# Kernel optimization log

Hardware: AMD Instinct MI355X
Metric: run time of the kernel (lower is better)

## Reference

```python
import jax, jax.numpy as jnp
import numpy as np

D_IN = 2048
D_OUT = 2048
NUM_HEADS = 16
HEAD_DIM = D_OUT // NUM_HEADS


def setup_inputs() -> dict:
    key = jax.random.key(0)
    k_x, k_qkv, k_proj, k_b = jax.random.split(key, 4)
    x = jax.random.normal(k_x, (2, 2048, D_IN), dtype=jnp.float32)
    # torch Linear(d_in, 3*d_out, bias=False): weight [3*d_out, d_in]; store transposed [d_in, 3*d_out]
    Wqkv = jax.random.normal(k_qkv, (D_IN, 3 * D_OUT), dtype=jnp.float32) / np.sqrt(D_IN)
    Wproj = jax.random.normal(k_proj, (D_OUT, D_OUT), dtype=jnp.float32) / np.sqrt(D_OUT)
    bproj = jax.random.normal(k_b, (D_OUT,), dtype=jnp.float32) * 0.01
    return {"x": x, "Wqkv": Wqkv, "Wproj": Wproj, "bproj": bproj}


def reference(x, Wqkv, Wproj, bproj):
    B, S, _ = x.shape
    qkv = x @ Wqkv  # [B, S, 3*D_OUT]
    qkv = qkv.reshape(B, S, 3, NUM_HEADS, HEAD_DIM)
    qkv = jnp.transpose(qkv, (2, 0, 3, 1, 4))  # [3, B, H, S, Dh]
    q, k, v = qkv[0], qkv[1], qkv[2]
    scale = 1.0 / np.sqrt(HEAD_DIM).astype(np.float32)
    scores = jnp.einsum('bhqd,bhkd->bhqk', q, k) * scale  # [B, H, S, S]
    causal = jnp.tril(jnp.ones((S, S), dtype=bool))
    scores = jnp.where(causal, scores, jnp.finfo(scores.dtype).min)
    attn = jax.nn.softmax(scores, axis=-1)
    out = jnp.einsum('bhqk,bhkd->bhqd', attn, v)  # [B, H, S, Dh]
    out = jnp.transpose(out, (0, 2, 1, 3)).reshape(B, S, D_OUT)
    return out @ Wproj + bproj
```

## Files before the change

kernel.cpp:

```cpp
#include <hip/hip_runtime.h>
#include <stdint.h>

typedef __attribute__((ext_vector_type(8))) short short8;
typedef __attribute__((ext_vector_type(4))) float f32x4;
typedef __attribute__((ext_vector_type(16))) float f32x16;
typedef __attribute__((ext_vector_type(4))) unsigned short u16x4;

typedef unsigned short u16;

constexpr int S_LEN = 2048;
constexpr int DH    = 128;

__device__ __forceinline__ u16 f2bf(float f) {
    union { float f; unsigned u; } v; v.f = f;
    unsigned r = v.u + 0x7FFFu + ((v.u >> 16) & 1u);
    return (u16)(r >> 16);
}
__device__ __forceinline__ void gl_lds16(const void* g, void* l) {
    __builtin_amdgcn_global_load_lds((const __attribute__((address_space(1))) void*)g,
                                     (__attribute__((address_space(3))) void*)l,
                                     16, 0, 0);
}

__global__ __launch_bounds__(256) void convx(const float* __restrict__ src,
                                             u16* __restrict__ dst) {
    size_t i = ((size_t)blockIdx.x * 256 + threadIdx.x) * 8;
    f32x4 a = *(const f32x4*)(src + i);
    f32x4 b = *(const f32x4*)(src + i + 4);
    short8 r;
    r[0] = (short)f2bf(a[0]); r[1] = (short)f2bf(a[1]);
    r[2] = (short)f2bf(a[2]); r[3] = (short)f2bf(a[3]);
    r[4] = (short)f2bf(b[0]); r[5] = (short)f2bf(b[1]);
    r[6] = (short)f2bf(b[2]); r[7] = (short)f2bf(b[3]);
    *(short8*)(dst + i) = r;
}

__global__ void convT(const float* __restrict__ src, u16* __restrict__ dst,
                      int rows, int cols) {
    __shared__ u16 tile[32][33];
    int c0 = blockIdx.x * 32, r0 = blockIdx.y * 32;
    int tx = threadIdx.x, ty = threadIdx.y;
#pragma unroll
    for (int i = 0; i < 32; i += 8)
        tile[ty + i][tx] = f2bf(src[(size_t)(r0 + ty + i) * cols + c0 + tx]);
    __syncthreads();
#pragma unroll
    for (int i = 0; i < 32; i += 8)
        dst[(size_t)(c0 + ty + i) * rows + r0 + tx] = tile[tx][ty + i];
}

__global__ __launch_bounds__(512, 2) void gemm_qkv(
        const u16* __restrict__ A, const u16* __restrict__ BT,
        u16* __restrict__ Qo, u16* __restrict__ Ko, u16* __restrict__ VTo) {
    __shared__ __align__(16) u16 lA[2][128 * 64];
    __shared__ __align__(16) u16 lB[2][256 * 64];
    const int tid = threadIdx.x;
    const int lane = tid & 63, wave = tid >> 6;
    const int quad = lane >> 4, l16 = lane & 15;
    const int wr = wave >> 2, wc = wave & 3;
    const int m0 = blockIdx.y * 128, n0 = blockIdx.x * 256;
    const int sw = l16 & 7;
    const int c4 = tid & 7;
    f32x4 acc[4][4] = {};

    auto stageA = [&](int t1, int nb) {
#pragma unroll
        for (int j = 0; j < 2; ++j) {
            int idx = j * 512 + tid;
            int row = idx >> 3;
            gl_lds16(A + (size_t)(m0 + row) * 2048 + t1 * 64 + ((c4 ^ (row & 7)) * 8),
                     &lA[nb][row * 64 + c4 * 8]);
        }
    };
    auto stageB = [&](int h, int t1, int nb) {
#pragma unroll
        for (int j = 0; j < 2; ++j) {
            int rih = (j * 512 + tid) >> 3;
            int row = (rih & 31) + h * 32 + (rih >> 5) * 64;
            gl_lds16(BT + (size_t)(n0 + row) * 2048 + t1 * 64 + ((c4 ^ (row & 7)) * 8),
                     &lB[nb][row * 64 + c4 * 8]);
        }
    };

    stageA(0, 0); stageB(0, 0, 0); stageB(1, 0, 0);

    constexpr int NT = 32;
    for (int t = 0; t < NT; ++t) {
        const int buf = t & 1, nb = buf ^ 1;
        const bool pf = (t + 1 < NT);
        asm volatile("s_waitcnt vmcnt(2)\n\ts_barrier" ::: "memory");
        short8 af[4][2], bf0[2][2];
        const int abase = (wr * 64 + l16) * 64;
        const int bbase = (wc * 64 + l16) * 64;
#pragma unroll
        for (int m = 0; m < 4; ++m)
#pragma unroll
            for (int ks = 0; ks < 2; ++ks)
                af[m][ks] = *(const short8*)&lA[buf][abase + m * 1024 + (((ks * 4 + quad) ^ sw)) * 8];
#pragma unroll
        for (int n = 0; n < 2; ++n)
#pragma unroll
            for (int ks = 0; ks < 2; ++ks)
                bf0[n][ks] = *(const short8*)&lB[buf][bbase + n * 1024 + (((ks * 4 + quad) ^ sw)) * 8];
        if (pf) { stageA(t + 1, nb); stageB(0, t + 1, nb); }
        __builtin_amdgcn_s_setprio(1);
#pragma unroll
        for (int m = 0; m < 4; ++m)
#pragma unroll
            for (int n = 0; n < 2; ++n)
#pragma unroll
                for (int ks = 0; ks < 2; ++ks)
                    acc[m][n] = __builtin_amdgcn_mfma_f32_16x16x32_bf16(
                        af[m][ks], bf0[n][ks], acc[m][n], 0, 0, 0);
        __builtin_amdgcn_s_setprio(0);
        if (pf) asm volatile("s_waitcnt vmcnt(4)\n\ts_barrier" ::: "memory");
        else    asm volatile("s_waitcnt vmcnt(0)\n\ts_barrier" ::: "memory");
        short8 bf1[2][2];
#pragma unroll
        for (int n = 0; n < 2; ++n)
#pragma unroll
            for (int ks = 0; ks < 2; ++ks)
                bf1[n][ks] = *(const short8*)&lB[buf][bbase + 2048 + n * 1024 + (((ks * 4 + quad) ^ sw)) * 8];
        if (pf) stageB(1, t + 1, nb);
        __builtin_amdgcn_s_setprio(1);
#pragma unroll
        for (int m = 0; m < 4; ++m)
#pragma unroll
            for (int n = 0; n < 2; ++n)
#pragma unroll
                for (int ks = 0; ks < 2; ++ks)
                    acc[m][n + 2] = __builtin_amdgcn_mfma_f32_16x16x32_bf16(
                        af[m][ks], bf1[n][ks], acc[m][n + 2], 0, 0, 0);
        __builtin_amdgcn_s_setprio(0);
    }

#pragma unroll
    for (int m = 0; m < 4; ++m) {
        int r0r = m0 + wr * 64 + m * 16 + quad * 4;
        int b = r0r >> 11, s0 = r0r & 2047;
#pragma unroll
        for (int n = 0; n < 4; ++n) {
            int cc = n0 + wc * 64 + n * 16 + l16;
            int which = cc >> 11, hd = (cc >> 7) & 15, dh = cc & 127;
            if (which < 2) {
                u16* dst = which == 0 ? Qo : Ko;
#pragma unroll
                for (int rg = 0; rg < 4; ++rg)
                    dst[(size_t)((b * 16 + hd) * 2048 + s0 + rg) * 128 + dh] = f2bf(acc[m][n][rg]);
            } else {
                u16x4 v;
#pragma unroll
                for (int rg = 0; rg < 4; ++rg) v[rg] = f2bf(acc[m][n][rg]);
                *(u16x4*)&VTo[((size_t)(b * 16 + hd) * 128 + dh) * 2048 + s0] = v;
            }
        }
    }
}

__global__ __launch_bounds__(256, 2) void attn_kern(
        u16* __restrict__ QOp, const u16* __restrict__ Kp,
        const u16* __restrict__ VTp) {
    __shared__ __align__(16) u16 lK[2][64 * 128];
    __shared__ __align__(16) u16 lV[2][128 * 64];
    const int tid = threadIdx.x, lane = tid & 63, wave = tid >> 6;
    const int ql = lane & 31, hi = lane >> 5;
    const int qb = (blockIdx.y < 8) ? (15 - (int)blockIdx.y) : ((int)blockIdx.y - 8);
    const int bh = blockIdx.x;
    const int qbase = qb * 128 + wave * 32;
    const int qmax = qbase + 31;
    const int nkt = 2 * qb + 2;
    u16* Qh = QOp + (size_t)bh * S_LEN * DH;
    const u16* Kh = Kp + (size_t)bh * S_LEN * DH;
    const u16* VTh = VTp + (size_t)bh * DH * S_LEN;

    short8 qf[8];
#pragma unroll
    for (int c = 0; c < 8; ++c)
        qf[c] = *(const short8*)&Qh[(size_t)(qbase + ql) * 128 + c * 16 + hi * 8];

    f32x16 acc[4] = {};
    float mrun = -1e30f, lrun = 0.f;
    const float SC = 0.08838834764831845f * 1.44269504088896f;

    auto stage = [&](int kt, int b) {
        const u16* ks = Kh + (size_t)kt * 64 * 128;
#pragma unroll
        for (int p = 0; p < 4; ++p) {
            int slot = p * 256 + tid;
            int row = slot >> 4, c4 = slot & 15;
            gl_lds16(ks + row * 128 + ((c4 ^ (row & 15)) * 8), &lK[b][slot * 8]);
        }
        const u16* vs = VTh + kt * 64;
#pragma unroll
        for (int p = 0; p < 4; ++p) {
            int slot = p * 256 + tid;
            int row = slot >> 3, c4 = slot & 7;
            gl_lds16(vs + (size_t)row * 2048 + ((c4 ^ (row & 7)) * 8), &lV[b][slot * 8]);
        }
    };

    stage(0, 0);
    __syncthreads();

    for (int kt = 0; kt < nkt; ++kt) {
        const int buf = kt & 1;
        if (kt + 1 < nkt) stage(kt + 1, buf ^ 1);
        if (kt * 64 <= qmax) {
            const bool part = (kt * 64 + 63 > qbase);
            f32x16 s0 = {}, s1 = {};
            __builtin_amdgcn_s_setprio(1);
#pragma unroll
            for (int c = 0; c < 8; ++c) {
                int sl = ((c * 2 + hi) ^ (ql & 15)) * 8;
                short8 k0 = *(const short8*)&lK[buf][ql * 128 + sl];
                short8 k1 = *(const short8*)&lK[buf][(32 + ql) * 128 + sl];
                s0 = __builtin_amdgcn_mfma_f32_32x32x16_bf16(k0, qf[c], s0, 0, 0, 0);
                s1 = __builtin_amdgcn_mfma_f32_32x32x16_bf16(k1, qf[c], s1, 0, 0, 0);
            }
            __builtin_amdgcn_s_setprio(0);
            float pv0[16], pv1[16];
            float pm = -1e30f;
            const int qg = qbase + ql;
#pragma unroll
            for (int r = 0; r < 16; ++r) {
                int krow = (r & 3) + 8 * (r >> 2) + 4 * hi;
                float a = s0[r] * SC;
                float b = s1[r] * SC;
                if (part) {
                    if (kt * 64 + krow > qg)      a = -1e30f;
                    if (kt * 64 + 32 + krow > qg) b = -1e30f;
                }
                pv0[r] = a; pv1[r] = b;
                pm = fmaxf(pm, fmaxf(a, b));
            }
            pm = fmaxf(pm, __shfl_xor(pm, 32));
            if (__any(pm - mrun > 8.f)) {
                float mn = fmaxf(mrun, pm);
                float al = exp2f(mrun - mn);
                mrun = mn;
                lrun *= al;
#pragma unroll
                for (int r = 0; r < 16; ++r) {
                    float ar = __shfl(al, (r & 3) + 8 * (r >> 2) + 4 * hi);
#pragma unroll
                    for (int dc = 0; dc < 4; ++dc)
                        acc[dc][r] *= ar;
                }
            }
            float rs = 0.f;
#pragma unroll
            for (int r = 0; r < 16; ++r) {
                pv0[r] = exp2f(pv0[r] - mrun);
                pv1[r] = exp2f(pv1[r] - mrun);
                rs += pv0[r] + pv1[r];
            }
            rs += __shfl_xor(rs, 32);
            lrun += rs;
            unsigned X0[8], X1[8];
#pragma unroll
            for (int i = 0; i < 8; ++i) {
                X0[i] = (unsigned)f2bf(pv0[2 * i]) | ((unsigned)f2bf(pv0[2 * i + 1]) << 16);
                X1[i] = (unsigned)f2bf(pv1[2 * i]) | ((unsigned)f2bf(pv1[2 * i + 1]) << 16);
            }
            short8 pa[4];
#pragma unroll
            for (int t = 0; t < 2; ++t)
#pragma unroll
                for (int h = 0; h < 2; ++h) {
                    unsigned x0 = t ? X1[4 * h + 0] : X0[4 * h + 0];
                    unsigned x1 = t ? X1[4 * h + 1] : X0[4 * h + 1];
                    unsigned x2 = t ? X1[4 * h + 2] : X0[4 * h + 2];
                    unsigned x3 = t ? X1[4 * h + 3] : X0[4 * h + 3];
                    unsigned sx0 = (unsigned)__shfl_xor((int)x0, 32);
                    unsigned sx1 = (unsigned)__shfl_xor((int)x1, 32);
                    unsigned sx2 = (unsigned)__shfl_xor((int)x2, 32);
                    unsigned sx3 = (unsigned)__shfl_xor((int)x3, 32);
                    union { unsigned u[4]; short8 s; } uf;
                    uf.u[0] = hi ? sx2 : x0;
                    uf.u[1] = hi ? sx3 : x1;
                    uf.u[2] = hi ? x2 : sx0;
                    uf.u[3] = hi ? x3 : sx1;
                    pa[t * 2 + h] = uf.s;
                }
            __builtin_amdgcn_s_setprio(1);
#pragma unroll
            for (int dc = 0; dc < 4; ++dc) {
                const int rv = dc * 32 + ql;
#pragma unroll
                for (int kc = 0; kc < 4; ++kc) {
                    short8 vf = *(const short8*)&lV[buf][rv * 64 + (((kc * 2 + hi) ^ (ql & 7)) * 8)];
                    acc[dc] = __builtin_amdgcn_mfma_f32_32x32x16_bf16(pa[kc], vf, acc[dc], 0, 0, 0);
                }
            }
            __builtin_amdgcn_s_setprio(0);
        }
        __syncthreads();
    }

    float linv = 1.f / lrun;
#pragma unroll
    for (int r = 0; r < 16; ++r) {
        int qr = (r & 3) + 8 * (r >> 2) + 4 * hi;
        float lr = __shfl(linv, qr);
        int qq = qbase + qr;
#pragma unroll
        for (int dc = 0; dc < 4; ++dc)
            Qh[(size_t)qq * 128 + dc * 32 + ql] = f2bf(acc[dc][r] * lr);
    }
}

__global__ __launch_bounds__(256) void gemm_proj(
        const u16* __restrict__ QO, const u16* __restrict__ BT,
        const float* __restrict__ bias, float* __restrict__ out) {
    __shared__ __align__(16) u16 lA[128 * 32];
    __shared__ __align__(16) u16 lB[128 * 32];
    const int tid = threadIdx.x;
    const int lane = tid & 63, wave = tid >> 6;
    const int quad = lane >> 4, l16 = lane & 15;
    const int wm = wave >> 1, wn = wave & 1;
    const int m0 = blockIdx.y * 128, n0 = blockIdx.x * 128;
    f32x4 acc[4][4] = {};
    const int rbase = tid >> 2;
    const int cofs  = (tid & 3) * 8;

    for (int k0 = 0; k0 < 2048; k0 += 32) {
#pragma unroll
        for (int it = 0; it < 2; ++it) {
            int row = m0 + it * 64 + rbase;
            int b = row >> 11, s = row & 2047;
            int k = k0 + cofs, h = k >> 7, dh = k & 127;
            gl_lds16(QO + ((size_t)(b * 16 + h) * 2048 + s) * 128 + dh, &lA[(it * 256 + tid) * 8]);
            gl_lds16(BT + (size_t)(n0 + it * 64 + rbase) * 2048 + k0 + cofs, &lB[(it * 256 + tid) * 8]);
        }
        __syncthreads();
        short8 af[4], bf[4];
#pragma unroll
        for (int i = 0; i < 4; ++i) {
            af[i] = *(const short8*)&lA[(wm * 64 + i * 16 + l16) * 32 + quad * 8];
            bf[i] = *(const short8*)&lB[(wn * 64 + i * 16 + l16) * 32 + quad * 8];
        }
#pragma unroll
        for (int im = 0; im < 4; ++im)
#pragma unroll
            for (int in = 0; in < 4; ++in)
                acc[im][in] = __builtin_amdgcn_mfma_f32_16x16x32_bf16(af[im], bf[in], acc[im][in], 0, 0, 0);
        __syncthreads();
    }
#pragma unroll
    for (int im = 0; im < 4; ++im) {
        int r0r = m0 + wm * 64 + im * 16 + quad * 4;
#pragma unroll
        for (int in = 0; in < 4; ++in) {
            int cc = n0 + wn * 64 + in * 16 + l16;
            float bv = bias[cc];
#pragma unroll
            for (int rg = 0; rg < 4; ++rg)
                out[(size_t)(r0r + rg) * 2048 + cc] = acc[im][in][rg] + bv;
        }
    }
}

extern "C" void kernel_launch(void* const* d_in, const int* in_sizes, int n_in,
                              void* d_out, int out_size, void* d_ws, size_t ws_size,
                              hipStream_t stream) {
    const float *x = nullptr, *Wqkv = nullptr, *Wproj = nullptr, *bproj = nullptr;
    for (int i = 0; i < n_in; ++i) {
        int sz = in_sizes[i];
        if      (sz == 2 * 2048 * 2048) x     = (const float*)d_in[i];
        else if (sz == 2048 * 6144)     Wqkv  = (const float*)d_in[i];
        else if (sz == 2048 * 2048)     Wproj = (const float*)d_in[i];
        else if (sz == 2048)            bproj = (const float*)d_in[i];
    }
    float* out = (float*)d_out;

    u16* xb     = (u16*)d_ws;
    u16* WqkvT  = xb    + (size_t)4096 * 2048;
    u16* Qb     = WqkvT + (size_t)6144 * 2048;
    u16* Kb     = Qb    + (size_t)32 * 2048 * 128;
    u16* VTb    = Kb    + (size_t)32 * 2048 * 128;
    u16* WprojT = xb;

    convx<<<dim3(4096), dim3(256), 0, stream>>>(x, xb);
    convT<<<dim3(192, 64), dim3(32, 8), 0, stream>>>(Wqkv, WqkvT, 2048, 6144);
    gemm_qkv<<<dim3(24, 32), dim3(512), 0, stream>>>(xb, WqkvT, Qb, Kb, VTb);
    convT<<<dim3(64, 64), dim3(32, 8), 0, stream>>>(Wproj, WprojT, 2048, 2048);
    attn_kern<<<dim3(32, 16), dim3(256), 0, stream>>>(Qb, Kb, VTb);
    gemm_proj<<<dim3(16, 32), dim3(256), 0, stream>>>(Qb, WprojT, bproj, out);
}
```

Measured before the change: 376.4 us.

## Load GEMM A fragments directly to registers, swizzle block order, upgrade proj GEMM

The QKV GEMM no longer stages A through LDS. It loads A fragments straight from global memory into double-buffered registers one tile ahead, and the vmcnt waits are adjusted to match. Both GEMMs now use a 1D grid with an XCD-aware block swizzle so that neighbouring tiles share L2. The projection GEMM is rewritten to reuse the pipelined 512-thread 128x256 double-buffered LDS design from the QKV GEMM. The register-direct A path gives up LDS reuse of A across waves and adds register pressure.

```diff
diff --git a/kernel.cpp b/kernel.cpp
--- a/kernel.cpp
+++ b/kernel.cpp
@@ -52,26 +52,19 @@
 __global__ __launch_bounds__(512, 2) void gemm_qkv(
         const u16* __restrict__ A, const u16* __restrict__ BT,
         u16* __restrict__ Qo, u16* __restrict__ Ko, u16* __restrict__ VTo) {
-    __shared__ __align__(16) u16 lA[2][128 * 64];
     __shared__ __align__(16) u16 lB[2][256 * 64];
     const int tid = threadIdx.x;
     const int lane = tid & 63, wave = tid >> 6;
     const int quad = lane >> 4, l16 = lane & 15;
     const int wr = wave >> 2, wc = wave & 3;
-    const int m0 = blockIdx.y * 128, n0 = blockIdx.x * 256;
+    const int bid = blockIdx.x;
+    const int swz = (bid & 7) * 96 + (bid >> 3);
+    const int m0 = (swz / 24) * 128, n0 = (swz % 24) * 256;
     const int sw = l16 & 7;
     const int c4 = tid & 7;
     f32x4 acc[4][4] = {};
-
-    auto stageA = [&](int t1, int nb) {
-#pragma unroll
-        for (int j = 0; j < 2; ++j) {
-            int idx = j * 512 + tid;
-            int row = idx >> 3;
-            gl_lds16(A + (size_t)(m0 + row) * 2048 + t1 * 64 + ((c4 ^ (row & 7)) * 8),
-                     &lA[nb][row * 64 + c4 * 8]);
-        }
-    };
+    constexpr int NT = 32;
+
     auto stageB = [&](int h, int t1, int nb) {
 #pragma unroll
         for (int j = 0; j < 2; ++j) {
@@ -81,28 +74,38 @@
                      &lB[nb][row * 64 + c4 * 8]);
         }
     };
-
-    stageA(0, 0); stageB(0, 0, 0); stageB(1, 0, 0);
-
-    constexpr int NT = 32;
-    for (int t = 0; t < NT; ++t) {
+    auto loadA = [&](int t1, short8 (&an)[4][2]) {
+#pragma unroll
+        for (int m = 0; m < 4; ++m)
+#pragma unroll
+            for (int ks = 0; ks < 2; ++ks)
+                an[m][ks] = *(const short8*)(A + (size_t)(m0 + wr * 64 + m * 16 + l16) * 2048
+                                               + t1 * 64 + (ks * 4 + quad) * 8);
+    };
+
+    short8 afA[4][2], afB[4][2];
+    stageB(0, 0, 0);
+    asm volatile("" ::: "memory");
+    loadA(0, afA);
+    asm volatile("" ::: "memory");
+    stageB(1, 0, 0);
+
+    auto tile_body = [&](int t, short8 (&ac)[4][2], short8 (&an)[4][2]) {
         const int buf = t & 1, nb = buf ^ 1;
         const bool pf = (t + 1 < NT);
-        asm volatile("s_waitcnt vmcnt(2)\n\ts_barrier" ::: "memory");
-        short8 af[4][2], bf0[2][2];
-        const int abase = (wr * 64 + l16) * 64;
+        asm volatile("s_waitcnt vmcnt(10)\n\ts_barrier" ::: "memory");
+        short8 bf0[2][2];
         const int bbase = (wc * 64 + l16) * 64;
 #pragma unroll
-        for (int m = 0; m < 4; ++m)
-#pragma unroll
-            for (int ks = 0; ks < 2; ++ks)
-                af[m][ks] = *(const short8*)&lA[buf][abase + m * 1024 + (((ks * 4 + quad) ^ sw)) * 8];
-#pragma unroll
         for (int n = 0; n < 2; ++n)
 #pragma unroll
             for (int ks = 0; ks < 2; ++ks)
                 bf0[n][ks] = *(const short8*)&lB[buf][bbase + n * 1024 + (((ks * 4 + quad) ^ sw)) * 8];
-        if (pf) { stageA(t + 1, nb); stageB(0, t + 1, nb); }
+        if (pf) stageB(0, t + 1, nb);
+        asm volatile("" ::: "memory");
+        if (pf) loadA(t + 1, an);
+        asm volatile("" ::: "memory");
+        if (pf) stageB(1, t + 1, nb);
         __builtin_amdgcn_s_setprio(1);
 #pragma unroll
         for (int m = 0; m < 4; ++m)
@@ -111,9 +114,9 @@
 #pragma unroll
                 for (int ks = 0; ks < 2; ++ks)
                     acc[m][n] = __builtin_amdgcn_mfma_f32_16x16x32_bf16(
-                        af[m][ks], bf0[n][ks], acc[m][n], 0, 0, 0);
+                        ac[m][ks], bf0[n][ks], acc[m][n], 0, 0, 0);
         __builtin_amdgcn_s_setprio(0);
-        if (pf) asm volatile("s_waitcnt vmcnt(4)\n\ts_barrier" ::: "memory");
+        if (pf) asm volatile("s_waitcnt vmcnt(12)\n\ts_barrier" ::: "memory");
         else    asm volatile("s_waitcnt vmcnt(0)\n\ts_barrier" ::: "memory");
         short8 bf1[2][2];
 #pragma unroll
@@ -121,7 +124,6 @@
 #pragma unroll
             for (int ks = 0; ks < 2; ++ks)
                 bf1[n][ks] = *(const short8*)&lB[buf][bbase + 2048 + n * 1024 + (((ks * 4 + quad) ^ sw)) * 8];
-        if (pf) stageB(1, t + 1, nb);
         __builtin_amdgcn_s_setprio(1);
 #pragma unroll
         for (int m = 0; m < 4; ++m)
@@ -130,8 +132,13 @@
 #pragma unroll
                 for (int ks = 0; ks < 2; ++ks)
                     acc[m][n + 2] = __builtin_amdgcn_mfma_f32_16x16x32_bf16(
-                        af[m][ks], bf1[n][ks], acc[m][n + 2], 0, 0, 0);
+                        ac[m][ks], bf1[n][ks], acc[m][n + 2], 0, 0, 0);
         __builtin_amdgcn_s_setprio(0);
+    };
+
+    for (int t2 = 0; t2 < NT; t2 += 2) {
+        tile_body(t2,     afA, afB);
+        tile_body(t2 + 1, afB, afA);
     }
 
 #pragma unroll
@@ -309,53 +316,106 @@
     }
 }
 
-__global__ __launch_bounds__(256) void gemm_proj(
+__global__ __launch_bounds__(512, 2) void gemm_proj(
         const u16* __restrict__ QO, const u16* __restrict__ BT,
         const float* __restrict__ bias, float* __restrict__ out) {
-    __shared__ __align__(16) u16 lA[128 * 32];
-    __shared__ __align__(16) u16 lB[128 * 32];
+    __shared__ __align__(16) u16 lA[2][128 * 64];
+    __shared__ __align__(16) u16 lB[2][256 * 64];
     const int tid = threadIdx.x;
     const int lane = tid & 63, wave = tid >> 6;
     const int quad = lane >> 4, l16 = lane & 15;
-    const int wm = wave >> 1, wn = wave & 1;
-    const int m0 = blockIdx.y * 128, n0 = blockIdx.x * 128;
+    const int wr = wave >> 2, wc = wave & 3;
+    const int bid = blockIdx.x;
+    const int swz = (bid & 7) * 32 + (bid >> 3);
+    const int m0 = (swz >> 3) * 128, n0 = (swz & 7) * 256;
+    const int sw = l16 & 7;
+    const int c4 = tid & 7;
     f32x4 acc[4][4] = {};
-    const int rbase = tid >> 2;
-    const int cofs  = (tid & 3) * 8;
-
-    for (int k0 = 0; k0 < 2048; k0 += 32) {
-#pragma unroll
-        for (int it = 0; it < 2; ++it) {
-            int row = m0 + it * 64 + rbase;
-            int b = row >> 11, s = row & 2047;
-            int k = k0 + cofs, h = k >> 7, dh = k & 127;
-            gl_lds16(QO + ((size_t)(b * 16 + h) * 2048 + s) * 128 + dh, &lA[(it * 256 + tid) * 8]);
-            gl_lds16(BT + (size_t)(n0 + it * 64 + rbase) * 2048 + k0 + cofs, &lB[(it * 256 + tid) * 8]);
-        }
-        __syncthreads();
-        short8 af[4], bf[4];
-#pragma unroll
-        for (int i = 0; i < 4; ++i) {
-            af[i] = *(const short8*)&lA[(wm * 64 + i * 16 + l16) * 32 + quad * 8];
-            bf[i] = *(const short8*)&lB[(wn * 64 + i * 16 + l16) * 32 + quad * 8];
-        }
-#pragma unroll
-        for (int im = 0; im < 4; ++im)
-#pragma unroll
-            for (int in = 0; in < 4; ++in)
-                acc[im][in] = __builtin_amdgcn_mfma_f32_16x16x32_bf16(af[im], bf[in], acc[im][in], 0, 0, 0);
-        __syncthreads();
-    }
-#pragma unroll
-    for (int im = 0; im < 4; ++im) {
-        int r0r = m0 + wm * 64 + im * 16 + quad * 4;
-#pragma unroll
-        for (int in = 0; in < 4; ++in) {
-            int cc = n0 + wn * 64 + in * 16 + l16;
+
+    auto stageA = [&](int t1, int nb) {
+#pragma unroll
+        for (int j = 0; j < 2; ++j) {
+            int row = (j * 512 + tid) >> 3;
+            int r = m0 + row;
+            int b = r >> 11, s = r & 2047;
+            int k = t1 * 64 + ((c4 ^ (row & 7)) * 8);
+            int h = k >> 7, dh = k & 127;
+            gl_lds16(QO + ((size_t)(b * 16 + h) * 2048 + s) * 128 + dh,
+                     &lA[nb][row * 64 + c4 * 8]);
+        }
+    };
+    auto stageB = [&](int h, int t1, int nb) {
+#pragma unroll
+        for (int j = 0; j < 2; ++j) {
+            int rih = (j * 512 + tid) >> 3;
+            int row = (rih & 31) + h * 32 + (rih >> 5) * 64;
+            gl_lds16(BT + (size_t)(n0 + row) * 2048 + t1 * 64 + ((c4 ^ (row & 7)) * 8),
+                     &lB[nb][row * 64 + c4 * 8]);
+        }
+    };
+
+    stageA(0, 0); stageB(0, 0, 0); stageB(1, 0, 0);
+
+    constexpr int NT = 32;
+    for (int t = 0; t < NT; ++t) {
+        const int buf = t & 1, nb = buf ^ 1;
+        const bool pf = (t + 1 < NT);
+        asm volatile("s_waitcnt vmcnt(2)\n\ts_barrier" ::: "memory");
+        short8 af[4][2], bf0[2][2];
+        const int abase = (wr * 64 + l16) * 64;
+        const int bbase = (wc * 64 + l16) * 64;
+#pragma unroll
+        for (int m = 0; m < 4; ++m)
+#pragma unroll
+            for (int ks = 0; ks < 2; ++ks)
+                af[m][ks] = *(const short8*)&lA[buf][abase + m * 1024 + (((ks * 4 + quad) ^ sw)) * 8];
+#pragma unroll
+        for (int n = 0; n < 2; ++n)
+#pragma unroll
+            for (int ks = 0; ks < 2; ++ks)
+                bf0[n][ks] = *(const short8*)&lB[buf][bbase + n * 1024 + (((ks * 4 + quad) ^ sw)) * 8];
+        if (pf) { stageA(t + 1, nb); stageB(0, t + 1, nb); }
+        __builtin_amdgcn_s_setprio(1);
+#pragma unroll
+        for (int m = 0; m < 4; ++m)
+#pragma unroll
+            for (int n = 0; n < 2; ++n)
+#pragma unroll
+                for (int ks = 0; ks < 2; ++ks)
+                    acc[m][n] = __builtin_amdgcn_mfma_f32_16x16x32_bf16(
+                        af[m][ks], bf0[n][ks], acc[m][n], 0, 0, 0);
+        __builtin_amdgcn_s_setprio(0);
+        if (pf) asm volatile("s_waitcnt vmcnt(4)\n\ts_barrier" ::: "memory");
+        else    asm volatile("s_waitcnt vmcnt(0)\n\ts_barrier" ::: "memory");
+        short8 bf1[2][2];
+#pragma unroll
+        for (int n = 0; n < 2; ++n)
+#pragma unroll
+            for (int ks = 0; ks < 2; ++ks)
+                bf1[n][ks] = *(const short8*)&lB[buf][bbase + 2048 + n * 1024 + (((ks * 4 + quad) ^ sw)) * 8];
+        if (pf) stageB(1, t + 1, nb);
+        __builtin_amdgcn_s_setprio(1);
+#pragma unroll
+        for (int m = 0; m < 4; ++m)
+#pragma unroll
+            for (int n = 0; n < 2; ++n)
+#pragma unroll
+                for (int ks = 0; ks < 2; ++ks)
+                    acc[m][n + 2] = __builtin_amdgcn_mfma_f32_16x16x32_bf16(
+                        af[m][ks], bf1[n][ks], acc[m][n + 2], 0, 0, 0);
+        __builtin_amdgcn_s_setprio(0);
+    }
+
+#pragma unroll
+    for (int m = 0; m < 4; ++m) {
+        int r0r = m0 + wr * 64 + m * 16 + quad * 4;
+#pragma unroll
+        for (int n = 0; n < 4; ++n) {
+            int cc = n0 + wc * 64 + n * 16 + l16;
             float bv = bias[cc];
 #pragma unroll
             for (int rg = 0; rg < 4; ++rg)
-                out[(size_t)(r0r + rg) * 2048 + cc] = acc[im][in][rg] + bv;
+                out[(size_t)(r0r + rg) * 2048 + cc] = acc[m][n][rg] + bv;
         }
     }
 }
@@ -382,8 +442,8 @@
 
     convx<<<dim3(4096), dim3(256), 0, stream>>>(x, xb);
     convT<<<dim3(192, 64), dim3(32, 8), 0, stream>>>(Wqkv, WqkvT, 2048, 6144);
-    gemm_qkv<<<dim3(24, 32), dim3(512), 0, stream>>>(xb, WqkvT, Qb, Kb, VTb);
+    gemm_qkv<<<dim3(768), dim3(512), 0, stream>>>(xb, WqkvT, Qb, Kb, VTb);
     convT<<<dim3(64, 64), dim3(32, 8), 0, stream>>>(Wproj, WprojT, 2048, 2048);
     attn_kern<<<dim3(32, 16), dim3(256), 0, stream>>>(Qb, Kb, VTb);
-    gemm_proj<<<dim3(16, 32), dim3(256), 0, stream>>>(Qb, WprojT, bproj, out);
-}
+    gemm_proj<<<dim3(256), dim3(512), 0, stream>>>(Qb, WprojT, bproj, out);
+}
```

Result: slower. 504.2 us (+33.9%).
